# Performance work log

Measured on AMD Instinct MI355X. Metric: run time of the kernel, lower is better.

## Reference

```python
import jax, jax.numpy as jnp
import numpy as np

B, S, IN, OUT = 4, 2048, 4096, 11008

def setup_inputs() -> dict:
    key = jax.random.key(0)
    k1, k2, k3, k4, k5 = jax.random.split(key, 5)
    x = jax.random.normal(k1, (B, S, IN), dtype=jnp.float32)
    # int8-range quantized weight stored as int32 for portability
    weight = jax.random.randint(k2, (OUT, IN), 0, 256, dtype=jnp.int32) - 128
    scale = (jax.random.uniform(k3, (OUT, 1), dtype=jnp.float32) * 0.01 + 1e-4).astype(jnp.float16)
    zp = jax.random.randint(k4, (OUT, 1), 0, 256, dtype=jnp.int32) - 128
    bias = jax.random.normal(k5, (OUT,), dtype=jnp.float32) * 0.02
    return {"x": x, "weight": weight, "scale": scale, "zp": zp, "bias": bias}

def reference(x, weight, scale, zp, bias):
    dtype = x.dtype
    # per-row dequant: (w_q - zp) * scale, then F.linear(x, w_rec, bias)
    w_rec = (weight.astype(dtype) - zp.astype(dtype)) * scale.astype(dtype)  # [OUT, IN]
    return jnp.einsum('bsi,oi->bso', x, w_rec) + bias
```

## Files before the change

kernel.cpp:

```cpp
#include <hip/hip_runtime.h>
#include <hip/hip_bf16.h>


#define MDIM 8192
#define NDIM 11008
#define KDIM 4096

#define BM 256
#define BN 256
#define BK 64
#define KT (KDIM / BK)
#define NTM (MDIM / BM)
#define NTN (NDIM / BN)
#define NWG (NTM * NTN)

typedef signed char i8;
typedef int i32x4 __attribute__((ext_vector_type(4)));


__global__ void conv_w8(const int* __restrict__ w, i8* __restrict__ w8) {
    const size_t e = ((size_t)blockIdx.x * 256 + threadIdx.x) << 4;
    const int4 a = *(const int4*)(w + e);
    const int4 b = *(const int4*)(w + e + 4);
    const int4 c = *(const int4*)(w + e + 8);
    const int4 d = *(const int4*)(w + e + 12);
    i8 q[16];
    q[0] = (i8)a.x; q[1] = (i8)a.y; q[2] = (i8)a.z; q[3] = (i8)a.w;
    q[4] = (i8)b.x; q[5] = (i8)b.y; q[6] = (i8)b.z; q[7] = (i8)b.w;
    q[8] = (i8)c.x; q[9] = (i8)c.y; q[10] = (i8)c.z; q[11] = (i8)c.w;
    q[12] = (i8)d.x; q[13] = (i8)d.y; q[14] = (i8)d.z; q[15] = (i8)d.w;
    *(int4*)(w8 + e) = *(const int4*)q;
}

__global__ __launch_bounds__(256) void conv_xq(const float* __restrict__ x,
                                               i8* __restrict__ xq,
                                               float* __restrict__ sx,
                                               float* __restrict__ xs) {
    __shared__ float ramax[4], rsum[4];
    const int row = blockIdx.x;
    const float* xr = x + (size_t)row * KDIM;
    const int t = threadIdx.x;
    const float4* p = (const float4*)xr + (t << 2);
    float4 v0 = p[0], v1 = p[1], v2 = p[2], v3 = p[3];
    float amax = 0.f, sum = 0.f;
    float vv[16] = {v0.x, v0.y, v0.z, v0.w, v1.x, v1.y, v1.z, v1.w,
                    v2.x, v2.y, v2.z, v2.w, v3.x, v3.y, v3.z, v3.w};
#pragma unroll
    for (int i = 0; i < 16; ++i) {
        amax = fmaxf(amax, fabsf(vv[i]));
        sum += vv[i];
    }
#pragma unroll
    for (int off = 32; off > 0; off >>= 1) {
        amax = fmaxf(amax, __shfl_down(amax, off, 64));
        sum += __shfl_down(sum, off, 64);
    }
    if ((t & 63) == 0) { ramax[t >> 6] = amax; rsum[t >> 6] = sum; }
    __syncthreads();
    amax = fmaxf(fmaxf(ramax[0], ramax[1]), fmaxf(ramax[2], ramax[3]));
    sum = (rsum[0] + rsum[1]) + (rsum[2] + rsum[3]);
    const float inv = (amax > 0.f) ? 127.0f / amax : 0.f;
    if (t == 0) {
        sx[row] = amax * (1.0f / 127.0f);
        xs[row] = sum;
    }
    i8 q[16];
#pragma unroll
    for (int i = 0; i < 16; ++i) q[i] = (i8)(int)rintf(vv[i] * inv);
    *(int4*)(xq + (size_t)row * KDIM + (t << 4)) = *(const int4*)q;
}


__device__ __forceinline__ void gload16(const i8* g, i8* l) {
    __builtin_amdgcn_global_load_lds(
        (const __attribute__((address_space(1))) unsigned int*)g,
        (__attribute__((address_space(3))) unsigned int*)l, 16, 0, 0);
}

#define STAGE_A(T) do { const int _s = (T) & 3; const int _k = (T) * BK;          \
    gload16(gA0 + _k, &SH[_s][0][wid * 1024]);                                    \
    gload16(gA1 + _k, &SH[_s][0][8192 + wid * 1024]); } while (0)
#define STAGE_B(T) do { const int _s = (T) & 3; const int _k = (T) * BK;          \
    gload16(gB0 + _k, &SH[_s][1][wid * 1024]);                                    \
    gload16(gB1 + _k, &SH[_s][1][8192 + wid * 1024]); } while (0)

#define GROUP(T, DO_STAGE, WAITOP) do {                                           \
    const i8* _sA = &SH[(T) & 3][0][0];                                           \
    const i8* _sB = &SH[(T) & 3][1][0];                                           \
    i32x4 aFr[8], bF[4];                                                          \
    _Pragma("unroll") for (int _f = 0; _f < 8; ++_f)                              \
        aFr[_f] = *(const i32x4*)(_sA + aoff + _f * 1024);                        \
    _Pragma("unroll") for (int _f = 0; _f < 4; ++_f)                              \
        bF[_f] = *(const i32x4*)(_sB + boff + _f * 1024);                         \
    if (DO_STAGE) { STAGE_A((T) + 3); STAGE_B((T) + 3); }                         \
    __builtin_amdgcn_s_barrier();                                                 \
    __builtin_amdgcn_s_setprio(1);                                                \
    _Pragma("unroll") for (int _i = 0; _i < 8; ++_i)                              \
    _Pragma("unroll") for (int _j = 0; _j < 4; ++_j)                              \
        acc[_i][_j] = __builtin_amdgcn_mfma_i32_16x16x64_i8(                      \
            aFr[_i], bF[_j], acc[_i][_j], 0, 0, 0);                               \
    __builtin_amdgcn_s_setprio(0);                                                \
    WAITOP;                                                                       \
    __builtin_amdgcn_s_barrier();                                                 \
} while (0)

__global__ __launch_bounds__(512, 2) void gemm_q(const i8* __restrict__ Xq,
                                                 const i8* __restrict__ Wq,
                                                 const float* __restrict__ sx,
                                                 const float* __restrict__ xs,
                                                 const float* __restrict__ scale,
                                                 const int* __restrict__ zp,
                                                 const float* __restrict__ bias,
                                                 float* __restrict__ out) {
    __shared__ __align__(16) i8 SH[4][2][16384];

    const int tid = threadIdx.x;
    const int wid = tid >> 6;
    const int lane = tid & 63;

    const int bid = blockIdx.x;
    const int pm = ((bid & 7) << 2) | ((bid >> 3) & 3);
    const int pn = bid >> 5;
    const int bm0 = pm * BM;
    const int bn0 = pn * BN;

    const int srow = tid >> 2;
    const int scol = ((tid & 3) << 4) ^ (((tid >> 5) & 1) << 5);
    const i8* gA0 = Xq + (size_t)(bm0 + srow) * KDIM + scol;
    const i8* gA1 = gA0 + (size_t)128 * KDIM;
    const i8* gB0 = Wq + (size_t)(bn0 + srow) * KDIM + scol;
    const i8* gB1 = gB0 + (size_t)128 * KDIM;

    const int wm = wid >> 2, wn = wid & 3;
    const int lr = lane & 15;
    const int kb = (lane >> 4) << 4;
    const int swz = (lr & 8) << 2;
    const int aoff = (((wm * 128 + lr) << 6) + kb) ^ swz;
    const int boff = (((wn * 64 + lr) << 6) + kb) ^ swz;

    i32x4 acc[8][4];
#pragma unroll
    for (int i = 0; i < 8; ++i)
#pragma unroll
        for (int j = 0; j < 4; ++j) acc[i][j] = (i32x4){0, 0, 0, 0};

    STAGE_A(0); STAGE_B(0);
    STAGE_A(1); STAGE_B(1);
    STAGE_A(2); STAGE_B(2);
    asm volatile("s_waitcnt vmcnt(8)" ::: "memory");
    __builtin_amdgcn_s_barrier();

    for (int t = 0; t < KT - 3; ++t) {
        GROUP(t, true, asm volatile("s_waitcnt vmcnt(8)" ::: "memory"));
    }
    GROUP(KT - 3, false, asm volatile("s_waitcnt vmcnt(4)" ::: "memory"));
    GROUP(KT - 2, false, asm volatile("s_waitcnt vmcnt(0)" ::: "memory"));
    GROUP(KT - 1, false, (void)0);

    const int rr = (lane >> 4) << 2;
#pragma unroll
    for (int j = 0; j < 4; ++j) {
        const int n = bn0 + wn * 64 + j * 16 + lr;
        const float sc = scale[n];
        const float zpn = (float)zp[n];
        const float bi = bias[n];
#pragma unroll
        for (int i = 0; i < 8; ++i) {
            const int m = bm0 + wm * 128 + i * 16 + rr;
#pragma unroll
            for (int r = 0; r < 4; ++r) {
                const int mm = m + r;
                const float d = (float)acc[i][j][r];
                out[(size_t)mm * NDIM + n] = sc * (sx[mm] * d - zpn * xs[mm]) + bi;
            }
        }
    }
}


__global__ void naive_q(const float* __restrict__ x, const int* __restrict__ wq,
                        const float* __restrict__ scale, const int* __restrict__ zp,
                        const float* __restrict__ bias, float* __restrict__ out) {
    const long long idx = (long long)blockIdx.x * 256 + threadIdx.x;
    if (idx >= (long long)MDIM * NDIM) return;
    const int m = (int)(idx / NDIM);
    const int n = (int)(idx % NDIM);
    const float* xr = x + (long long)m * KDIM;
    const int* wr = wq + (long long)n * KDIM;
    float dot = 0.f, xsum = 0.f;
    for (int k = 0; k < KDIM; ++k) {
        dot += xr[k] * (float)wr[k];
        xsum += xr[k];
    }
    out[idx] = scale[n] * (dot - (float)zp[n] * xsum) + bias[n];
}

extern "C" void kernel_launch(void* const* d_in, const int* in_sizes, int n_in,
                              void* d_out, int out_size, void* d_ws, size_t ws_size,
                              hipStream_t stream) {
    const float* x = (const float*)d_in[0];
    const int* wq = (const int*)d_in[1];
    const float* scale = (const float*)d_in[2];
    const int* zp = (const int*)d_in[3];
    const float* bias = (const float*)d_in[4];
    float* out = (float*)d_out;

    const size_t w8_bytes = (size_t)NDIM * KDIM;
    const size_t xq_bytes = (size_t)MDIM * KDIM;
    const size_t row_bytes = (size_t)MDIM * 4;
    const size_t need = w8_bytes + xq_bytes + 2 * row_bytes;

    if (ws_size >= need) {
        i8* w8 = (i8*)d_ws;
        i8* xq8 = (i8*)((char*)d_ws + w8_bytes);
        float* sx = (float*)((char*)d_ws + w8_bytes + xq_bytes);
        float* xs = (float*)((char*)d_ws + w8_bytes + xq_bytes + row_bytes);
        conv_w8<<<(unsigned)(w8_bytes / 16 / 256), 256, 0, stream>>>(wq, w8);
        conv_xq<<<MDIM, 256, 0, stream>>>(x, xq8, sx, xs);
        gemm_q<<<NWG, 512, 0, stream>>>(xq8, w8, sx, xs, scale, zp, bias, out);
    } else {
        const long long total = (long long)MDIM * NDIM;
        naive_q<<<(unsigned)((total + 255) / 256), 256, 0, stream>>>(
            x, wq, scale, zp, bias, out);
    }
}
```

Baseline: 578.3 us.

## Register double-buffer LDS fragments and use a three-stage ring with one barrier

The shared-memory ring goes from four K stages to three, and the fragment loads are double-buffered in registers. Each iteration issues the global-to-LDS prefetch for tile t+3 and the LDS reads for tile t+1, then runs the MFMAs on tile t from registers. It waits only once per iteration (vmcnt plus lgkmcnt) before a single barrier, instead of two barriers per tile. The aim is to hide LDS read latency behind the matrix ops and halve barrier overhead. The cost is doubled fragment registers, which could spill or hurt occupancy under the (512,2) launch bound.

```diff
diff --git a/kernel.cpp b/kernel.cpp
--- a/kernel.cpp
+++ b/kernel.cpp
@@ -77,32 +77,39 @@
         (__attribute__((address_space(3))) unsigned int*)l, 16, 0, 0);
 }
 
-#define STAGE_A(T) do { const int _s = (T) & 3; const int _k = (T) * BK;          \
+#define STAGE(T) do { const int _s = (T) % 3; const size_t _k = (size_t)(T) * BK; \
     gload16(gA0 + _k, &SH[_s][0][wid * 1024]);                                    \
-    gload16(gA1 + _k, &SH[_s][0][8192 + wid * 1024]); } while (0)
-#define STAGE_B(T) do { const int _s = (T) & 3; const int _k = (T) * BK;          \
+    gload16(gA1 + _k, &SH[_s][0][8192 + wid * 1024]);                             \
     gload16(gB0 + _k, &SH[_s][1][wid * 1024]);                                    \
     gload16(gB1 + _k, &SH[_s][1][8192 + wid * 1024]); } while (0)
 
-#define GROUP(T, DO_STAGE, WAITOP) do {                                           \
-    const i8* _sA = &SH[(T) & 3][0][0];                                           \
-    const i8* _sB = &SH[(T) & 3][1][0];                                           \
-    i32x4 aFr[8], bF[4];                                                          \
+#define READS(T, FA, FB) do {                                                     \
+    const i8* _sA = &SH[(T) % 3][0][0];                                           \
+    const i8* _sB = &SH[(T) % 3][1][0];                                           \
     _Pragma("unroll") for (int _f = 0; _f < 8; ++_f)                              \
-        aFr[_f] = *(const i32x4*)(_sA + aoff + _f * 1024);                        \
+        FA[_f] = *(const i32x4*)(_sA + aoff + _f * 1024);                         \
     _Pragma("unroll") for (int _f = 0; _f < 4; ++_f)                              \
-        bF[_f] = *(const i32x4*)(_sB + boff + _f * 1024);                         \
-    if (DO_STAGE) { STAGE_A((T) + 3); STAGE_B((T) + 3); }                         \
-    __builtin_amdgcn_s_barrier();                                                 \
+        FB[_f] = *(const i32x4*)(_sB + boff + _f * 1024); } while (0)
+
+#define MFMAS(FA, FB) do {                                                        \
     __builtin_amdgcn_s_setprio(1);                                                \
     _Pragma("unroll") for (int _i = 0; _i < 8; ++_i)                              \
     _Pragma("unroll") for (int _j = 0; _j < 4; ++_j)                              \
         acc[_i][_j] = __builtin_amdgcn_mfma_i32_16x16x64_i8(                      \
-            aFr[_i], bF[_j], acc[_i][_j], 0, 0, 0);                               \
-    __builtin_amdgcn_s_setprio(0);                                                \
-    WAITOP;                                                                       \
-    __builtin_amdgcn_s_barrier();                                                 \
-} while (0)
+            FA[_i], FB[_j], acc[_i][_j], 0, 0, 0);                                \
+    __builtin_amdgcn_s_setprio(0); } while (0)
+
+#define VM4 asm volatile("s_waitcnt vmcnt(4)" ::: "memory")
+#define VM0 asm volatile("s_waitcnt vmcnt(0)" ::: "memory")
+#define LG0 asm volatile("s_waitcnt lgkmcnt(0)" ::: "memory")
+
+#define GROUPX(T, FAc, FBc, FAn, FBn, DO_STAGE, DO_READ, WAIT) do {               \
+    if (DO_STAGE) STAGE((T) + 3);                                                 \
+    if (DO_READ) READS((T) + 1, FAn, FBn);                                        \
+    MFMAS(FAc, FBc);                                                              \
+    WAIT;                                                                         \
+    LG0;                                                                          \
+    __builtin_amdgcn_s_barrier(); } while (0)
 
 __global__ __launch_bounds__(512, 2) void gemm_q(const i8* __restrict__ Xq,
                                                  const i8* __restrict__ Wq,
@@ -112,7 +119,7 @@
                                                  const int* __restrict__ zp,
                                                  const float* __restrict__ bias,
                                                  float* __restrict__ out) {
-    __shared__ __align__(16) i8 SH[4][2][16384];
+    __shared__ __align__(16) i8 SH[3][2][16384];
 
     const int tid = threadIdx.x;
     const int wid = tid >> 6;
@@ -144,18 +151,24 @@
 #pragma unroll
         for (int j = 0; j < 4; ++j) acc[i][j] = (i32x4){0, 0, 0, 0};
 
-    STAGE_A(0); STAGE_B(0);
-    STAGE_A(1); STAGE_B(1);
-    STAGE_A(2); STAGE_B(2);
+    i32x4 FA0[8], FB0[4], FA1[8], FB1[4];
+
+    STAGE(0); STAGE(1); STAGE(2);
     asm volatile("s_waitcnt vmcnt(8)" ::: "memory");
     __builtin_amdgcn_s_barrier();
-
-    for (int t = 0; t < KT - 3; ++t) {
-        GROUP(t, true, asm volatile("s_waitcnt vmcnt(8)" ::: "memory"));
-    }
-    GROUP(KT - 3, false, asm volatile("s_waitcnt vmcnt(4)" ::: "memory"));
-    GROUP(KT - 2, false, asm volatile("s_waitcnt vmcnt(0)" ::: "memory"));
-    GROUP(KT - 1, false, (void)0);
+    READS(0, FA0, FB0);
+    LG0;
+    VM4;
+    __builtin_amdgcn_s_barrier();
+
+    for (int t = 0; t < 60; t += 2) {
+        GROUPX(t,     FA0, FB0, FA1, FB1, true, true, VM4);
+        GROUPX(t + 1, FA1, FB1, FA0, FB0, true, true, VM4);
+    }
+    GROUPX(60, FA0, FB0, FA1, FB1, true,  true,  VM4);
+    GROUPX(61, FA1, FB1, FA0, FB0, false, true,  VM0);
+    GROUPX(62, FA0, FB0, FA1, FB1, false, true,  (void)0);
+    GROUPX(63, FA1, FB1, FA0, FB0, false, false, (void)0);
 
     const int rr = (lane >> 4) << 2;
 #pragma unroll
```

Result: faster. 565.9 us (-2.1%).

## Split GEMM k-step into four interleaved phases and fuse prep kernels

Applied to the files above, without the earlier changes.

The main loop of the int8 GEMM now processes two k-tiles per iteration. Each k-tile is split into four phases that interleave partial LDS fragment reads, single global-to-LDS loads and quarter-sized MFMA batches, with barriers between phases. The intent is to overlap LDS reads and global loads with matrix work at finer granularity and to lower register pressure from fragments. The two preprocessing kernels are merged into one launch to save a launch. The extra barriers per tile add synchronisation overhead.

```diff
diff --git a/kernel.cpp b/kernel.cpp
--- a/kernel.cpp
+++ b/kernel.cpp
@@ -18,56 +18,58 @@
 typedef int i32x4 __attribute__((ext_vector_type(4)));
 
 
-__global__ void conv_w8(const int* __restrict__ w, i8* __restrict__ w8) {
-    const size_t e = ((size_t)blockIdx.x * 256 + threadIdx.x) << 4;
-    const int4 a = *(const int4*)(w + e);
-    const int4 b = *(const int4*)(w + e + 4);
-    const int4 c = *(const int4*)(w + e + 8);
-    const int4 d = *(const int4*)(w + e + 12);
-    i8 q[16];
-    q[0] = (i8)a.x; q[1] = (i8)a.y; q[2] = (i8)a.z; q[3] = (i8)a.w;
-    q[4] = (i8)b.x; q[5] = (i8)b.y; q[6] = (i8)b.z; q[7] = (i8)b.w;
-    q[8] = (i8)c.x; q[9] = (i8)c.y; q[10] = (i8)c.z; q[11] = (i8)c.w;
-    q[12] = (i8)d.x; q[13] = (i8)d.y; q[14] = (i8)d.z; q[15] = (i8)d.w;
-    *(int4*)(w8 + e) = *(const int4*)q;
-}
-
-__global__ __launch_bounds__(256) void conv_xq(const float* __restrict__ x,
-                                               i8* __restrict__ xq,
-                                               float* __restrict__ sx,
-                                               float* __restrict__ xs) {
-    __shared__ float ramax[4], rsum[4];
-    const int row = blockIdx.x;
-    const float* xr = x + (size_t)row * KDIM;
+__global__ __launch_bounds__(256) void prep(const float* __restrict__ x,
+                                            const int* __restrict__ w,
+                                            i8* __restrict__ xq,
+                                            float* __restrict__ sx,
+                                            float* __restrict__ xs,
+                                            i8* __restrict__ w8) {
     const int t = threadIdx.x;
-    const float4* p = (const float4*)xr + (t << 2);
-    float4 v0 = p[0], v1 = p[1], v2 = p[2], v3 = p[3];
-    float amax = 0.f, sum = 0.f;
-    float vv[16] = {v0.x, v0.y, v0.z, v0.w, v1.x, v1.y, v1.z, v1.w,
-                    v2.x, v2.y, v2.z, v2.w, v3.x, v3.y, v3.z, v3.w};
-#pragma unroll
-    for (int i = 0; i < 16; ++i) {
-        amax = fmaxf(amax, fabsf(vv[i]));
-        sum += vv[i];
-    }
-#pragma unroll
-    for (int off = 32; off > 0; off >>= 1) {
-        amax = fmaxf(amax, __shfl_down(amax, off, 64));
-        sum += __shfl_down(sum, off, 64);
-    }
-    if ((t & 63) == 0) { ramax[t >> 6] = amax; rsum[t >> 6] = sum; }
-    __syncthreads();
-    amax = fmaxf(fmaxf(ramax[0], ramax[1]), fmaxf(ramax[2], ramax[3]));
-    sum = (rsum[0] + rsum[1]) + (rsum[2] + rsum[3]);
-    const float inv = (amax > 0.f) ? 127.0f / amax : 0.f;
-    if (t == 0) {
-        sx[row] = amax * (1.0f / 127.0f);
-        xs[row] = sum;
-    }
-    i8 q[16];
-#pragma unroll
-    for (int i = 0; i < 16; ++i) q[i] = (i8)(int)rintf(vv[i] * inv);
-    *(int4*)(xq + (size_t)row * KDIM + (t << 4)) = *(const int4*)q;
+    if (blockIdx.x < MDIM) {
+        __shared__ float ramax[4], rsum[4];
+        const int row = blockIdx.x;
+        const float* xr = x + (size_t)row * KDIM;
+        const float4* p = (const float4*)xr + (t << 2);
+        float4 v0 = p[0], v1 = p[1], v2 = p[2], v3 = p[3];
+        float amax = 0.f, sum = 0.f;
+        float vv[16] = {v0.x, v0.y, v0.z, v0.w, v1.x, v1.y, v1.z, v1.w,
+                        v2.x, v2.y, v2.z, v2.w, v3.x, v3.y, v3.z, v3.w};
+#pragma unroll
+        for (int i = 0; i < 16; ++i) {
+            amax = fmaxf(amax, fabsf(vv[i]));
+            sum += vv[i];
+        }
+#pragma unroll
+        for (int off = 32; off > 0; off >>= 1) {
+            amax = fmaxf(amax, __shfl_down(amax, off, 64));
+            sum += __shfl_down(sum, off, 64);
+        }
+        if ((t & 63) == 0) { ramax[t >> 6] = amax; rsum[t >> 6] = sum; }
+        __syncthreads();
+        amax = fmaxf(fmaxf(ramax[0], ramax[1]), fmaxf(ramax[2], ramax[3]));
+        sum = (rsum[0] + rsum[1]) + (rsum[2] + rsum[3]);
+        const float inv = (amax > 0.f) ? 127.0f / amax : 0.f;
+        if (t == 0) {
+            sx[row] = amax * (1.0f / 127.0f);
+            xs[row] = sum;
+        }
+        i8 q[16];
+#pragma unroll
+        for (int i = 0; i < 16; ++i) q[i] = (i8)(int)rintf(vv[i] * inv);
+        *(int4*)(xq + (size_t)row * KDIM + (t << 4)) = *(const int4*)q;
+    } else {
+        const size_t e = (((size_t)(blockIdx.x - MDIM) * 256 + t) << 4);
+        const int4 a = *(const int4*)(w + e);
+        const int4 b = *(const int4*)(w + e + 4);
+        const int4 c = *(const int4*)(w + e + 8);
+        const int4 d = *(const int4*)(w + e + 12);
+        i8 q[16];
+        q[0] = (i8)a.x; q[1] = (i8)a.y; q[2] = (i8)a.z; q[3] = (i8)a.w;
+        q[4] = (i8)b.x; q[5] = (i8)b.y; q[6] = (i8)b.z; q[7] = (i8)b.w;
+        q[8] = (i8)c.x; q[9] = (i8)c.y; q[10] = (i8)c.z; q[11] = (i8)c.w;
+        q[12] = (i8)d.x; q[13] = (i8)d.y; q[14] = (i8)d.z; q[15] = (i8)d.w;
+        *(int4*)(w8 + e) = *(const int4*)q;
+    }
 }
 
 
@@ -77,31 +79,55 @@
         (__attribute__((address_space(3))) unsigned int*)l, 16, 0, 0);
 }
 
-#define STAGE_A(T) do { const int _s = (T) & 3; const int _k = (T) * BK;          \
-    gload16(gA0 + _k, &SH[_s][0][wid * 1024]);                                    \
-    gload16(gA1 + _k, &SH[_s][0][8192 + wid * 1024]); } while (0)
-#define STAGE_B(T) do { const int _s = (T) & 3; const int _k = (T) * BK;          \
-    gload16(gB0 + _k, &SH[_s][1][wid * 1024]);                                    \
-    gload16(gB1 + _k, &SH[_s][1][8192 + wid * 1024]); } while (0)
-
-#define GROUP(T, DO_STAGE, WAITOP) do {                                           \
-    const i8* _sA = &SH[(T) & 3][0][0];                                           \
-    const i8* _sB = &SH[(T) & 3][1][0];                                           \
-    i32x4 aFr[8], bF[4];                                                          \
-    _Pragma("unroll") for (int _f = 0; _f < 8; ++_f)                              \
-        aFr[_f] = *(const i32x4*)(_sA + aoff + _f * 1024);                        \
-    _Pragma("unroll") for (int _f = 0; _f < 4; ++_f)                              \
-        bF[_f] = *(const i32x4*)(_sB + boff + _f * 1024);                         \
-    if (DO_STAGE) { STAGE_A((T) + 3); STAGE_B((T) + 3); }                         \
-    __builtin_amdgcn_s_barrier();                                                 \
-    __builtin_amdgcn_s_setprio(1);                                                \
-    _Pragma("unroll") for (int _i = 0; _i < 8; ++_i)                              \
-    _Pragma("unroll") for (int _j = 0; _j < 4; ++_j)                              \
-        acc[_i][_j] = __builtin_amdgcn_mfma_i32_16x16x64_i8(                      \
-            aFr[_i], bF[_j], acc[_i][_j], 0, 0, 0);                               \
-    __builtin_amdgcn_s_setprio(0);                                                \
-    WAITOP;                                                                       \
-    __builtin_amdgcn_s_barrier();                                                 \
+#define SG(T, IDX) do { const int _s = (T) & 3; const size_t _k = (size_t)(T) * BK; \
+    if ((IDX) == 0)      gload16(gA0 + _k, &SH[_s][0][wid * 1024]);                 \
+    else if ((IDX) == 1) gload16(gA1 + _k, &SH[_s][0][8192 + wid * 1024]);          \
+    else if ((IDX) == 2) gload16(gB0 + _k, &SH[_s][1][wid * 1024]);                 \
+    else                 gload16(gB1 + _k, &SH[_s][1][8192 + wid * 1024]); } while (0)
+
+#define SLOTA(T) (&SH[(T) & 3][0][0])
+#define SLOTB(T) (&SH[(T) & 3][1][0])
+
+#define RD1(T) do { const i8* _sA = SLOTA(T); const i8* _sB = SLOTB(T);            \
+    _Pragma("unroll") for (int _f = 0; _f < 4; ++_f)                               \
+        a0[_f] = *(const i32x4*)(_sA + aoff + _f * 1024);                          \
+    _Pragma("unroll") for (int _j = 0; _j < 2; ++_j)                               \
+        b01[_j] = *(const i32x4*)(_sB + boff + _j * 1024); } while (0)
+
+#define RD2(T) do { const i8* _sB = SLOTB(T);                                      \
+    _Pragma("unroll") for (int _j = 0; _j < 2; ++_j)                               \
+        b23[_j] = *(const i32x4*)(_sB + boff + (_j + 2) * 1024); } while (0)
+
+#define RD3(T) do { const i8* _sA = SLOTA(T);                                      \
+    _Pragma("unroll") for (int _f = 0; _f < 4; ++_f)                               \
+        a1[_f] = *(const i32x4*)(_sA + aoff + (_f + 4) * 1024); } while (0)
+
+#define MQ(AF, BF, IOFF, JOFF) do {                                                \
+    _Pragma("unroll") for (int _i = 0; _i < 4; ++_i)                               \
+    _Pragma("unroll") for (int _j = 0; _j < 2; ++_j)                               \
+        acc[_i + (IOFF)][_j + (JOFF)] = __builtin_amdgcn_mfma_i32_16x16x64_i8(     \
+            AF[_i], BF[_j], acc[_i + (IOFF)][_j + (JOFF)], 0, 0, 0); } while (0)
+
+#define NOPX ((void)0)
+#define VM4 asm volatile("s_waitcnt vmcnt(4)" ::: "memory")
+#define VM0 asm volatile("s_waitcnt vmcnt(0)" ::: "memory")
+
+#define PH(RDS, STG, MMS, TWS) do { RDS; STG;                                      \
+    __builtin_amdgcn_s_barrier();                                                  \
+    asm volatile("s_waitcnt lgkmcnt(0)" ::: "memory");                             \
+    __builtin_amdgcn_s_setprio(1); MMS; __builtin_amdgcn_s_setprio(0);             \
+    TWS; __builtin_amdgcn_s_barrier(); } while (0)
+
+#define PAIR(T, SA, SB, W4, W8) do {                                               \
+    i32x4 a0[4], a1[4], b01[2], b23[2];                                            \
+    PH(RD1(T), if (SA) { SG((T) + 3, 0); }, MQ(a0, b01, 0, 0), NOPX);              \
+    PH(RD2(T), if (SA) { SG((T) + 3, 1); }, MQ(a0, b23, 0, 2), NOPX);              \
+    PH(RD3(T), if (SA) { SG((T) + 3, 2); }, MQ(a1, b01, 4, 0), NOPX);              \
+    PH(NOPX,   if (SA) { SG((T) + 3, 3); }, MQ(a1, b23, 4, 2), W4);                \
+    PH(RD1((T) + 1), if (SB) { SG((T) + 4, 0); }, MQ(a0, b01, 0, 0), NOPX);        \
+    PH(RD2((T) + 1), if (SB) { SG((T) + 4, 1); }, MQ(a0, b23, 0, 2), NOPX);        \
+    PH(RD3((T) + 1), if (SB) { SG((T) + 4, 2); }, MQ(a1, b01, 4, 0), NOPX);        \
+    PH(NOPX,         if (SB) { SG((T) + 4, 3); }, MQ(a1, b23, 4, 2), W8);          \
 } while (0)
 
 __global__ __launch_bounds__(512, 2) void gemm_q(const i8* __restrict__ Xq,
@@ -144,18 +170,17 @@
 #pragma unroll
         for (int j = 0; j < 4; ++j) acc[i][j] = (i32x4){0, 0, 0, 0};
 
-    STAGE_A(0); STAGE_B(0);
-    STAGE_A(1); STAGE_B(1);
-    STAGE_A(2); STAGE_B(2);
+    SG(0, 0); SG(0, 1); SG(0, 2); SG(0, 3);
+    SG(1, 0); SG(1, 1); SG(1, 2); SG(1, 3);
+    SG(2, 0); SG(2, 1); SG(2, 2); SG(2, 3);
     asm volatile("s_waitcnt vmcnt(8)" ::: "memory");
     __builtin_amdgcn_s_barrier();
 
-    for (int t = 0; t < KT - 3; ++t) {
-        GROUP(t, true, asm volatile("s_waitcnt vmcnt(8)" ::: "memory"));
-    }
-    GROUP(KT - 3, false, asm volatile("s_waitcnt vmcnt(4)" ::: "memory"));
-    GROUP(KT - 2, false, asm volatile("s_waitcnt vmcnt(0)" ::: "memory"));
-    GROUP(KT - 1, false, (void)0);
+    for (int p = 0; p < 30; ++p) {
+        PAIR(2 * p, true, true, VM4, VM4);
+    }
+    PAIR(60, true, false, VM4, VM0);
+    PAIR(62, false, false, NOPX, NOPX);
 
     const int rr = (lane >> 4) << 2;
 #pragma unroll
@@ -215,8 +240,7 @@
         i8* xq8 = (i8*)((char*)d_ws + w8_bytes);
         float* sx = (float*)((char*)d_ws + w8_bytes + xq_bytes);
         float* xs = (float*)((char*)d_ws + w8_bytes + xq_bytes + row_bytes);
-        conv_w8<<<(unsigned)(w8_bytes / 16 / 256), 256, 0, stream>>>(wq, w8);
-        conv_xq<<<MDIM, 256, 0, stream>>>(x, xq8, sx, xs);
+        prep<<<MDIM + NDIM, 256, 0, stream>>>(x, wq, xq8, sx, xs, w8);
         gemm_q<<<NWG, 512, 0, stream>>>(xq8, w8, sx, xs, scale, zp, bias, out);
     } else {
         const long long total = (long long)MDIM * NDIM;
```

After: 551.1 us. 1.05x faster.
